# Optimization experiments

Hardware: AMD Instinct MI355X
Metric: run time of the kernel (lower is better)

The kernel has to match this reference:

```python
import jax, jax.numpy as jnp
import numpy as np
import math

D_MODEL = 1024
N_HEADS = 16
C = 1
B, L = 8, 2048


def _glorot(key, fan):
    lim = np.sqrt(6.0 / (fan + fan)).astype(np.float32)
    return jax.random.uniform(key, (fan, fan), jnp.float32, -lim, lim)


def setup_inputs() -> dict:
    key = jax.random.key(0)
    ks = jax.random.split(key, 7)
    queries = jax.random.normal(ks[0], (B, L, D_MODEL), jnp.float32)
    keys = jax.random.normal(ks[1], (B, L, D_MODEL), jnp.float32)
    values = jax.random.normal(ks[2], (B, L, D_MODEL), jnp.float32)
    wq = _glorot(ks[3], D_MODEL)
    wk = _glorot(ks[4], D_MODEL)
    wv = _glorot(ks[5], D_MODEL)
    wo = _glorot(ks[6], D_MODEL)
    return {"queries": queries, "keys": keys, "values": values,
            "wq": wq, "wk": wk, "wv": wv, "wo": wo}


def reference(queries, keys, values, wq, wk, wv, wo):
    Bv, Lv, _ = queries.shape
    H = N_HEADS
    Dh = D_MODEL // N_HEADS
    # Projections, then (B, L, H, Dh) -> (B, H, Dh, L)  (time axis last)
    Q = (queries @ wq).reshape(Bv, Lv, H, Dh).transpose(0, 2, 3, 1)
    K = (keys @ wk).reshape(Bv, Lv, H, Dh).transpose(0, 2, 3, 1)
    V = (values @ wv).reshape(Bv, Lv, H, Dh).transpose(0, 2, 3, 1)
    # FFT-based autocorrelation over the time axis, per (B,H,Dh) lane
    corr = jnp.fft.irfft(jnp.fft.rfft(Q, axis=-1) * jnp.conj(jnp.fft.rfft(K, axis=-1)), n=Lv, axis=-1)  # (B,H,Dh,L)
    k_top = int(math.floor(C * math.log(Lv)))
    top_vals, top_idx = jax.lax.top_k(corr, k_top)          # (B,H,Dh,k)
    w = jax.nn.softmax(top_vals, axis=-1)                    # (B,H,Dh,k)
    # Faithful to original roll_function: it rolls along the Dh axis
    # (which the source mislabels as seq_len), shifts taken mod Dh.
    # out[b,h,t,:] = V[b,h,(t - tau[b,h,t]) % Dh, :]
    t = jnp.arange(Dh)
    out = jnp.zeros_like(V)
    for i in range(k_top):  # small static loop (k_top = 7)
        gather_idx = (t[None, None, :] - top_idx[..., i]) % Dh   # (B,H,Dh)
        rolled = jnp.take_along_axis(V, gather_idx[..., None], axis=2)  # (B,H,Dh,L)
        out = out + w[..., i, None] * rolled
    # Faithful layout-scrambling reshape: (B,H,Dh,L)->(B,Dh,H,L)->(B,L,d_model)
    out = out.transpose(0, 2, 1, 3).reshape(Bv, Lv, D_MODEL)
    return out @ wo
```

## Files before the change

### kernel.cpp

```cpp
#include <hip/hip_runtime.h>
#include <math.h>

#define NB 8
#define NL 2048
#define ND 1024
#define NH 16
#define KTOP 7

typedef __attribute__((ext_vector_type(4))) float f32x4;
typedef __attribute__((ext_vector_type(8))) short s16x8;
typedef __attribute__((ext_vector_type(8))) _Float16 f16x8;
typedef __attribute__((ext_vector_type(4))) _Float16 f16x4;

__device__ __forceinline__ unsigned short f2bf(float x) {
  unsigned u = __float_as_uint(x);
  u = (u + 0x7FFFu + ((u >> 16) & 1u)) >> 16;
  return (unsigned short)u;
}
__device__ __forceinline__ float bf2f(unsigned short h) {
  return __uint_as_float(((unsigned)h) << 16);
}
__device__ __forceinline__ unsigned cvtpk_bf16(float a, float b) {
  unsigned d;
  asm("v_cvt_pk_bf16_f32 %0, %1, %2" : "=v"(d) : "v"(a), "v"(b));
  return d;
}
__device__ __forceinline__ float lo16(unsigned h) { return __uint_as_float(h << 16); }
__device__ __forceinline__ float hi16(unsigned h) { return __uint_as_float(h & 0xffff0000u); }

__device__ __forceinline__ void gll16(const void* g, void* l) {
  __builtin_amdgcn_global_load_lds(
      (const __attribute__((address_space(1))) void*)g,
      (__attribute__((address_space(3))) void*)l, 16, 0, 0);
}

__device__ __forceinline__ void asplit_write(float4 x, float4 y, short* ah, short* al, int wi) {
  unsigned h0 = cvtpk_bf16(x.x, x.y);
  unsigned h1 = cvtpk_bf16(x.z, x.w);
  unsigned h2 = cvtpk_bf16(y.x, y.y);
  unsigned h3 = cvtpk_bf16(y.z, y.w);
  float r0 = x.x - lo16(h0), r1 = x.y - hi16(h0);
  float r2 = x.z - lo16(h1), r3 = x.w - hi16(h1);
  float r4 = y.x - lo16(h2), r5 = y.y - hi16(h2);
  float r6 = y.z - lo16(h3), r7 = y.w - hi16(h3);
  unsigned l0 = cvtpk_bf16(r0, r1);
  unsigned l1 = cvtpk_bf16(r2, r3);
  unsigned l2 = cvtpk_bf16(r4, r5);
  unsigned l3 = cvtpk_bf16(r6, r7);
  *(uint4*)(ah + wi) = make_uint4(h0, h1, h2, h3);
  *(uint4*)(al + wi) = make_uint4(l0, l1, l2, l3);
}

__global__ __launch_bounds__(256) void wprep_kernel(
    const float* __restrict__ w0, const float* __restrict__ w1,
    const float* __restrict__ w2, const float* __restrict__ w3,
    short* __restrict__ wsplit, _Float16* __restrict__ wf16) {
  __shared__ float tile[32][33];
  int y = blockIdx.y;
  const float* in = (y == 0) ? w0 : (y == 1) ? w1 : (y == 2) ? w2 : w3;
  int bx = blockIdx.x & 31, by = blockIdx.x >> 5;
  int tx = threadIdx.x & 31, ty = threadIdx.x >> 5;
#pragma unroll
  for (int i = 0; i < 4; ++i)
    tile[ty + i * 8][tx] = in[(size_t)(by * 32 + ty + i * 8) * ND + bx * 32 + tx];
  __syncthreads();
#pragma unroll
  for (int i = 0; i < 4; ++i) {
    float x = tile[tx][ty + i * 8];
    int n = bx * 32 + ty + i * 8;
    int k = by * 32 + tx;
    if (y < 2) {
      short* oh = wsplit + (size_t)(2 * y) * ND * ND;
      short* ol = wsplit + (size_t)(2 * y + 1) * ND * ND;
      unsigned short h = f2bf(x);
      unsigned short l = f2bf(x - bf2f(h));
      size_t o = (size_t)n * ND + (k ^ (((n >> 1) & 3) << 3));
      oh[o] = (short)h;
      ol[o] = (short)l;
    } else {
      _Float16* of = wf16 + (size_t)(y - 2) * ND * ND;
      of[(size_t)n * ND + (k ^ ((n & 7) << 3))] = (_Float16)x;
    }
  }
}

__global__ __launch_bounds__(256) void gemm_split(
    const float* __restrict__ A, const short* __restrict__ BhT,
    const short* __restrict__ BlT, float* __restrict__ Ct) {
  constexpr int K = 1024;
  __shared__ short smem[32768];
  int t = threadIdx.x;
  int wg = (blockIdx.x & 7) * 128 + (blockIdx.x >> 3);
  int m0 = (wg >> 3) << 7, n0 = (wg & 7) << 7;
  int lane = t & 63;
  int wm = (t >> 7) & 1, wn = (t >> 6) & 1;
  int lrow = lane & 15, lk8 = (lane >> 4) << 3;

  int r0 = t >> 2, r1 = r0 + 64;
  int c8 = (t & 3) << 3;
  int wi0 = r0 * 32 + (c8 ^ (((r0 >> 1) & 3) << 3));
  int wi1 = r1 * 32 + (c8 ^ (((r1 >> 1) & 3) << 3));
  int lo0 = (t & 192) * 8;
  int lo1 = 2048 + (t & 192) * 8;

  const float* pa0 = A + (size_t)(m0 + r0) * K + c8;
  const float* pa1 = A + (size_t)(m0 + r1) * K + c8;
  const short* pb0h = BhT + (size_t)(n0 + r0) * K + c8;
  const short* pb1h = BhT + (size_t)(n0 + r1) * K + c8;
  const short* pb0l = BlT + (size_t)(n0 + r0) * K + c8;
  const short* pb1l = BlT + (size_t)(n0 + r1) * K + c8;

  int iA[4], iB[4];
#pragma unroll
  for (int f = 0; f < 4; ++f) {
    int ra = wm * 64 + f * 16 + lrow;
    iA[f] = ra * 32 + (lk8 ^ (((ra >> 1) & 3) << 3));
    int rb = wn * 64 + f * 16 + lrow;
    iB[f] = rb * 32 + (lk8 ^ (((rb >> 1) & 3) << 3));
  }

  f32x4 acc[4][4] = {};

  float4 sx0 = *(const float4*)(pa0);
  float4 sy0 = *(const float4*)(pa0 + 4);
  float4 sx1 = *(const float4*)(pa1);
  float4 sy1 = *(const float4*)(pa1 + 4);
  gll16(pb0h, smem + 8192 + lo0);
  gll16(pb1h, smem + 8192 + lo1);
  gll16(pb0l, smem + 12288 + lo0);
  gll16(pb1l, smem + 12288 + lo1);
  asplit_write(sx0, sy0, smem, smem + 4096, wi0);
  asplit_write(sx1, sy1, smem, smem + 4096, wi1);
  __syncthreads();

  for (int k0 = 0; k0 < K; k0 += 32) {
    short* cb = smem + ((k0 >> 5) & 1) * 16384;
    short* nb = smem + ((((k0 >> 5) & 1) ^ 1) * 16384);
    bool more = (k0 + 32) < K;
    if (more) {
      sx0 = *(const float4*)(pa0 + k0 + 32);
      sy0 = *(const float4*)(pa0 + k0 + 36);
      sx1 = *(const float4*)(pa1 + k0 + 32);
      sy1 = *(const float4*)(pa1 + k0 + 36);
      gll16(pb0h + k0 + 32, nb + 8192 + lo0);
      gll16(pb1h + k0 + 32, nb + 8192 + lo1);
      gll16(pb0l + k0 + 32, nb + 12288 + lo0);
      gll16(pb1l + k0 + 32, nb + 12288 + lo1);
    }
    s16x8 afh[4], afl[4];
#pragma unroll
    for (int mf = 0; mf < 4; ++mf) {
      afh[mf] = *(const s16x8*)(cb + iA[mf]);
      afl[mf] = *(const s16x8*)(cb + 4096 + iA[mf]);
    }
#pragma unroll
    for (int nf = 0; nf < 4; ++nf) {
      s16x8 bfh = *(const s16x8*)(cb + 8192 + iB[nf]);
      s16x8 bfl = *(const s16x8*)(cb + 12288 + iB[nf]);
#pragma unroll
      for (int mf = 0; mf < 4; ++mf)
        acc[mf][nf] = __builtin_amdgcn_mfma_f32_16x16x32_bf16(afh[mf], bfh, acc[mf][nf], 0, 0, 0);
#pragma unroll
      for (int mf = 0; mf < 4; ++mf)
        acc[mf][nf] = __builtin_amdgcn_mfma_f32_16x16x32_bf16(afh[mf], bfl, acc[mf][nf], 0, 0, 0);
#pragma unroll
      for (int mf = 0; mf < 4; ++mf)
        acc[mf][nf] = __builtin_amdgcn_mfma_f32_16x16x32_bf16(afl[mf], bfh, acc[mf][nf], 0, 0, 0);
    }
    if (more) {
      asplit_write(sx0, sy0, nb, nb + 4096, wi0);
      asplit_write(sx1, sy1, nb, nb + 4096, wi1);
    }
    __syncthreads();
  }

  int b = m0 >> 11;
  int mlbase = (m0 & 2047) + wm * 64 + (lane >> 4) * 4;
#pragma unroll
  for (int nf = 0; nf < 4; ++nf) {
    int n = n0 + wn * 64 + nf * 16 + lrow;
    float* rowp = Ct + ((size_t)(b * ND + n)) * NL + mlbase;
#pragma unroll
    for (int mf = 0; mf < 4; ++mf)
      *(float4*)(rowp + mf * 16) = *(float4*)&acc[mf][nf];
  }
}

template <int OUTMODE, bool AF32>
__global__ __launch_bounds__(256) void gemm_f16(
    const void* __restrict__ Av, const _Float16* __restrict__ BT,
    void* __restrict__ Cv) {
  constexpr int K = 1024;
  __shared__ _Float16 sA[8192];
  __shared__ _Float16 sB[8192];
  int t = threadIdx.x;
  int wg = (blockIdx.x & 7) * 128 + (blockIdx.x >> 3);
  int m0 = (wg >> 3) << 7, n0 = (wg & 7) << 7;
  int lane = t & 63;
  int wm = (t >> 7) & 1, wn = (t >> 6) & 1;
  int lrow = lane & 15, lk = (lane >> 4) << 3;

  f32x4 acc[4][4] = {};

  for (int k0 = 0; k0 < K; k0 += 64) {
#pragma unroll
    for (int it = 0; it < 4; ++it) {
      int e = it * 256 + t;
      int r = e >> 3, c8 = (e & 7) << 3;
      int lo = it * 2048 + (t & 192) * 8;
      gll16(BT + (size_t)(n0 + r) * K + k0 + c8, sB + lo);
      if (!AF32) {
        const _Float16* Af = (const _Float16*)Av;
        gll16(Af + (size_t)(m0 + r) * K + k0 + c8, sA + lo);
      }
    }
    if (AF32) {
      const float* Af = (const float*)Av;
#pragma unroll
      for (int it = 0; it < 4; ++it) {
        int ca = it * 256 + t;
        int r = ca >> 3, c8 = (ca & 7) << 3;
        const float* pa = Af + (size_t)(m0 + r) * K + k0 + c8;
        float4 x = *(const float4*)pa;
        float4 y = *(const float4*)(pa + 4);
        f16x8 o;
        o[0] = (_Float16)x.x; o[1] = (_Float16)x.y; o[2] = (_Float16)x.z; o[3] = (_Float16)x.w;
        o[4] = (_Float16)y.x; o[5] = (_Float16)y.y; o[6] = (_Float16)y.z; o[7] = (_Float16)y.w;
        *(f16x8*)(sA + r * 64 + (c8 ^ ((r & 7) << 3))) = o;
      }
    }
    __syncthreads();
#pragma unroll
    for (int kk = 0; kk < 64; kk += 32) {
      f16x8 af[4];
#pragma unroll
      for (int mf = 0; mf < 4; ++mf) {
        int row = wm * 64 + mf * 16 + lrow;
        af[mf] = *(const f16x8*)(sA + row * 64 + ((kk + lk) ^ ((row & 7) << 3)));
      }
#pragma unroll
      for (int nf = 0; nf < 4; ++nf) {
        int row = wn * 64 + nf * 16 + lrow;
        f16x8 bf = *(const f16x8*)(sB + row * 64 + ((kk + lk) ^ ((row & 7) << 3)));
#pragma unroll
        for (int mf = 0; mf < 4; ++mf)
          acc[mf][nf] = __builtin_amdgcn_mfma_f32_16x16x32_f16(af[mf], bf, acc[mf][nf], 0, 0, 0);
      }
    }
    __syncthreads();
  }

  if (OUTMODE == 0) {
    _Float16* C = (_Float16*)Cv;
    int b = m0 >> 11;
    int ml = (m0 & 2047) + wm * 64 + (lane >> 4) * 4;
#pragma unroll
    for (int nf = 0; nf < 4; ++nf) {
      int n = n0 + wn * 64 + nf * 16 + lrow;
      _Float16* row = C + ((size_t)(b * ND + n)) * NL + ml;
#pragma unroll
      for (int mf = 0; mf < 4; ++mf) {
        f16x4 v;
        v[0] = (_Float16)acc[mf][nf][0];
        v[1] = (_Float16)acc[mf][nf][1];
        v[2] = (_Float16)acc[mf][nf][2];
        v[3] = (_Float16)acc[mf][nf][3];
        *(f16x4*)(row + mf * 16) = v;
      }
    }
  } else {
    float* C = (float*)Cv;
#pragma unroll
    for (int mf = 0; mf < 4; ++mf)
#pragma unroll
      for (int nf = 0; nf < 4; ++nf) {
        int row = m0 + wm * 64 + mf * 16 + (lane >> 4) * 4;
        int col = n0 + wn * 64 + nf * 16 + lrow;
#pragma unroll
        for (int r = 0; r < 4; ++r)
          C[(size_t)(row + r) * ND + col] = acc[mf][nf][r];
      }
  }
}

__device__ __forceinline__ int SW(int i) { return i ^ ((i >> 4) & 7); }

__device__ __forceinline__ float2 cadd2(float2 a, float2 b) { return make_float2(a.x + b.x, a.y + b.y); }
__device__ __forceinline__ float2 csub2(float2 a, float2 b) { return make_float2(a.x - b.x, a.y - b.y); }
__device__ __forceinline__ float2 cmul2(float2 a, float2 b) {
  return make_float2(a.x * b.x - a.y * b.y, a.x * b.y + a.y * b.x);
}
__device__ __forceinline__ float2 cjs2(float2 a, float s) { return make_float2(-s * a.y, s * a.x); }
__device__ __forceinline__ float2 wtw(float rev) {
  return make_float2(__builtin_amdgcn_cosf(rev), __builtin_amdgcn_sinf(rev));
}

__device__ __forceinline__ void dft4(float2& b0, float2& b1, float2& b2, float2& b3, float s) {
  float2 t0 = cadd2(b0, b2), t1 = csub2(b0, b2);
  float2 t2 = cadd2(b1, b3), t3 = cjs2(csub2(b1, b3), s);
  b0 = cadd2(t0, t2);
  b1 = cadd2(t1, t3);
  b2 = csub2(t0, t2);
  b3 = csub2(t1, t3);
}

__device__ __forceinline__ void dft8(float2 a[8], float s) {
  float2 e0 = a[0], e1 = a[2], e2 = a[4], e3 = a[6];
  float2 o0 = a[1], o1 = a[3], o2 = a[5], o3 = a[7];
  dft4(e0, e1, e2, e3, s);
  dft4(o0, o1, o2, o3, s);
  const float c = 0.70710678118654752f;
  float2 w1 = make_float2(c, s * c);
  float2 w3 = make_float2(-c, s * c);
  o1 = cmul2(o1, w1);
  o2 = cjs2(o2, s);
  o3 = cmul2(o3, w3);
  a[0] = cadd2(e0, o0);
  a[4] = csub2(e0, o0);
  a[1] = cadd2(e1, o1);
  a[5] = csub2(e1, o1);
  a[2] = cadd2(e2, o2);
  a[6] = csub2(e2, o2);
  a[3] = cadd2(e3, o3);
  a[7] = csub2(e3, o3);
}

template <int LS>
__device__ __forceinline__ void pass8(const float2* __restrict__ in, float2* __restrict__ out,
                                      float s, int t) {
  float2 a[8];
  const float2* ip = in + (t ^ ((t >> 4) & 7));
#pragma unroll
  for (int r = 0; r < 8; ++r) a[r] = ip[256 * r];
  int k = t & (LS - 1);
  if (LS > 1) {
    float kf = s * (1.0f / (LS * 8)) * (float)k;
    float2 w1 = wtw(kf);
    float2 w4 = wtw(4.0f * kf);
    float2 w2 = cmul2(w1, w1);
    float2 w3 = cmul2(w2, w1);
    float2 w5 = cmul2(w4, w1);
    float2 w6 = cmul2(w4, w2);
    float2 w7 = cmul2(w4, w3);
    a[1] = cmul2(a[1], w1);
    a[2] = cmul2(a[2], w2);
    a[3] = cmul2(a[3], w3);
    a[4] = cmul2(a[4], w4);
    a[5] = cmul2(a[5], w5);
    a[6] = cmul2(a[6], w6);
    a[7] = cmul2(a[7], w7);
  }
  dft8(a, s);
  int ob = (t / LS) * (LS * 8) + k;
#pragma unroll
  for (int r = 0; r < 8; ++r) out[SW(ob + LS * r)] = a[r];
}

__global__ __launch_bounds__(256) void fft_topk_kernel(
    const float* __restrict__ Qt, const float* __restrict__ Kt,
    float* __restrict__ topw, int* __restrict__ topi) {
  __shared__ float2 X[2048];
  __shared__ float2 Y[2048];
  __shared__ float cv[2][4];
  __shared__ int ct[2][4];

  int t = threadIdx.x;
  size_t rix = blockIdx.x;
  const float* q = Qt + rix * NL;
  const float* k = Kt + rix * NL;

#pragma unroll
  for (int it = 0; it < 2; ++it) {
    int i0 = 4 * t + 1024 * it;
    float4 vq = *(const float4*)(q + i0);
    float4 vk = *(const float4*)(k + i0);
    int swb = SW(i0);
    X[swb ^ 0] = make_float2(vq.x, vk.x);
    X[swb ^ 1] = make_float2(vq.y, vk.y);
    X[swb ^ 2] = make_float2(vq.z, vk.z);
    X[swb ^ 3] = make_float2(vq.w, vk.w);
  }
  __syncthreads();

  pass8<1>(X, Y, -1.0f, t);
  __syncthreads();
  pass8<8>(Y, X, -1.0f, t);
  __syncthreads();
  pass8<64>(X, Y, -1.0f, t);
  __syncthreads();
#pragma unroll
  for (int h = 0; h < 2; ++h) {
    int b = t + 256 * h;
    float2 a[4];
    const float2* yp = Y + SW(b);
#pragma unroll
    for (int r = 0; r < 4; ++r) a[r] = yp[512 * r];
    float2 w = wtw(-(1.0f / 2048.0f) * (float)b);
    float2 w2 = cmul2(w, w);
    a[1] = cmul2(a[1], w);
    a[2] = cmul2(a[2], w2);
    a[3] = cmul2(a[3], cmul2(w2, w));
    dft4(a[0], a[1], a[2], a[3], -1.0f);
    float2* xp = X + SW(b);
#pragma unroll
    for (int r = 0; r < 4; ++r) xp[512 * r] = a[r];
  }
  __syncthreads();

#pragma unroll
  for (int it = 0; it < 8; ++it) {
    int f = t + 256 * it;
    int nf = (2048 - f) & 2047;
    float2 zf = X[SW(t) + 256 * it];
    float2 zn = X[SW(nf)];
    float a = zf.x, b2 = zf.y, c = zn.x, d = zn.y;
    float p = 0.5f * (a + c), qq = 0.5f * (b2 - d);
    float r2 = 0.5f * (b2 + d), s2 = -0.5f * (a - c);
    Y[SW(t) + 256 * it] = make_float2((p * r2 + qq * s2) * (1.0f / 2048.0f),
                                      (qq * r2 - p * s2) * (1.0f / 2048.0f));
  }
  __syncthreads();

  pass8<1>(Y, X, 1.0f, t);
  __syncthreads();
  pass8<8>(X, Y, 1.0f, t);
  __syncthreads();
  pass8<64>(Y, X, 1.0f, t);
  __syncthreads();

  float lv[8];
  int lt[8];
#pragma unroll
  for (int h = 0; h < 2; ++h) {
    int b = t + 256 * h;
    float2 a[4];
    const float2* xp = X + SW(b);
#pragma unroll
    for (int r = 0; r < 4; ++r) a[r] = xp[512 * r];
    float2 w = wtw((1.0f / 2048.0f) * (float)b);
    float2 w2 = cmul2(w, w);
    a[1] = cmul2(a[1], w);
    a[2] = cmul2(a[2], w2);
    a[3] = cmul2(a[3], cmul2(w2, w));
    dft4(a[0], a[1], a[2], a[3], 1.0f);
#pragma unroll
    for (int r = 0; r < 4; ++r) {
      lv[h * 4 + r] = a[r].x;
      lt[h * 4 + r] = b + 512 * r;
    }
  }

  int lane = t & 63, wave = t >> 6;
  float bv = lv[0];
  int bt = lt[0];
#pragma unroll
  for (int j = 1; j < 8; ++j)
    if (lv[j] > bv) { bv = lv[j]; bt = lt[j]; }

  float sel_v[KTOP];
  int sel_t[KTOP];
#pragma unroll
  for (int pass = 0; pass < KTOP; ++pass) {
    float rv = bv;
    int rt = bt;
#pragma unroll
    for (int m = 1; m < 64; m <<= 1) {
      float ov = __shfl_xor(rv, m, 64);
      int ot = __shfl_xor(rt, m, 64);
      if (ov > rv) { rv = ov; rt = ot; }
    }
    if (lane == 0) { cv[pass & 1][wave] = rv; ct[pass & 1][wave] = rt; }
    __syncthreads();
    float fv = cv[pass & 1][0];
    int ft = ct[pass & 1][0];
#pragma unroll
    for (int w = 1; w < 4; ++w) {
      float ov = cv[pass & 1][w];
      if (ov > fv) { fv = ov; ft = ct[pass & 1][w]; }
    }
    sel_v[pass] = fv;
    sel_t[pass] = ft;
    if (bt == ft) {
#pragma unroll
      for (int j = 0; j < 8; ++j)
        if (lt[j] == ft) lv[j] = -3.0e38f;
      bv = lv[0];
      bt = lt[0];
#pragma unroll
      for (int j = 1; j < 8; ++j)
        if (lv[j] > bv) { bv = lv[j]; bt = lt[j]; }
    }
  }

  if (t == 0) {
    float m = sel_v[0], ssum = 0.f, w[KTOP];
#pragma unroll
    for (int i = 0; i < KTOP; ++i) { w[i] = expf(sel_v[i] - m); ssum += w[i]; }
#pragma unroll
    for (int i = 0; i < KTOP; ++i) {
      topw[rix * KTOP + i] = w[i] / ssum;
      topi[rix * KTOP + i] = sel_t[i];
    }
  }
}

__global__ __launch_bounds__(256) void roll_kernel(
    const _Float16* __restrict__ V, const float* __restrict__ topw,
    const int* __restrict__ topi, _Float16* __restrict__ out) {
  __shared__ float vt[64][68];
  __shared__ float ws[64][8];
  __shared__ int ts[64][8];
  int blk = blockIdx.x;
  int b = blk >> 9;
  int h = (blk >> 5) & 15;
  int lc = blk & 31;
  int t = threadIdx.x;

#pragma unroll
  for (int it = 0; it < 2; ++it) {
    int e = it * 256 + t;
    int d = e >> 3, c8 = (e & 7) << 3;
    f16x8 v = *(const f16x8*)(V + ((size_t)(b * ND + h * 64 + d)) * NL + lc * 64 + c8);
#pragma unroll
    for (int j = 0; j < 8; ++j) vt[d][c8 + j] = (float)v[j];
  }
  for (int e = t; e < 64 * KTOP; e += 256) {
    int d = e / KTOP, i = e % KTOP;
    size_t rix = ((size_t)(b * 16 + h)) * 64 + d;
    ws[d][i] = topw[rix * KTOP + i];
    ts[d][i] = topi[rix * KTOP + i] & 63;
  }
  __syncthreads();

  int hi = lc >> 4;
  int c0 = (lc & 15) * 64;
#pragma unroll
  for (int it = 0; it < 16; ++it) {
    int e = it * 256 + t;
    int d = e >> 6, r = e & 63;
    float s = 0.f;
#pragma unroll
    for (int i = 0; i < KTOP; ++i) s += ws[d][i] * vt[(d - ts[d][i]) & 63][r];
    int rowp = d * 32 + h * 2 + hi;
    int col = c0 + r;
    out[((size_t)(b * NL + rowp)) * ND + (col ^ ((rowp & 7) << 3))] = (_Float16)s;
  }
}

extern "C" void kernel_launch(void* const* d_in, const int* in_sizes, int n_in,
                              void* d_out, int out_size, void* d_ws, size_t ws_size,
                              hipStream_t stream) {
  (void)in_sizes; (void)n_in; (void)out_size; (void)ws_size;
  const float* queries = (const float*)d_in[0];
  const float* keys    = (const float*)d_in[1];
  const float* values  = (const float*)d_in[2];
  const float* wq = (const float*)d_in[3];
  const float* wk = (const float*)d_in[4];
  const float* wv = (const float*)d_in[5];
  const float* wo = (const float*)d_in[6];
  float* outp = (float*)d_out;

  const size_t MB = 1024 * 1024;
  char* ws = (char*)d_ws;
  short*    wsplit = (short*)ws;
  _Float16* wf16   = (_Float16*)(ws + 8 * MB);
  float*    Qt     = (float*)(ws + 12 * MB);
  float*    Kt     = (float*)(ws + 76 * MB);
  float*    topw   = (float*)(ws + 140 * MB);
  int*      topi   = (int*)(ws + 140 * MB + (size_t)8192 * KTOP * 4);

  short* wqh = wsplit + (size_t)0 * ND * ND;
  short* wql = wsplit + (size_t)1 * ND * ND;
  short* wkh = wsplit + (size_t)2 * ND * ND;
  short* wkl = wsplit + (size_t)3 * ND * ND;
  _Float16* wv16 = wf16 + (size_t)0 * ND * ND;
  _Float16* wo16 = wf16 + (size_t)1 * ND * ND;

  _Float16* Vp = (_Float16*)Qt;
  _Float16* Xs = (_Float16*)Kt;

  wprep_kernel<<<dim3(1024, 4), 256, 0, stream>>>(wq, wk, wv, wo, wsplit, wf16);

  gemm_split<<<1024, 256, 0, stream>>>(queries, wqh, wql, Qt);
  gemm_split<<<1024, 256, 0, stream>>>(keys, wkh, wkl, Kt);

  fft_topk_kernel<<<8192, 256, 0, stream>>>(Qt, Kt, topw, topi);

  gemm_f16<0, true><<<1024, 256, 0, stream>>>(values, wv16, Vp);

  roll_kernel<<<NB * NH * 32, 256, 0, stream>>>(Vp, topw, topi, Xs);

  gemm_f16<2, false><<<1024, 256, 0, stream>>>(Xs, wo16, outp);
}
```

Measured before the change: 467.1 us.

## Double-buffer GEMM shared-memory tiles and fuse spectrum product into first FFT pass

The f16 GEMM kernel now ping-pongs between two shared-memory stages. The next K-tile's global loads (and, for fp32 A, the register-held values converted after the MFMAs) are issued while the current tile is being multiplied, and one barrier per iteration is dropped. Shared memory grows to 64 KB per block, which may reduce occupancy. Separately, the FFT correlation kernel computes the conjugate-product spectrum straight into registers and applies the first radix-8 pass in place, removing one LDS round trip and one barrier.

```diff
diff --git a/kernel.cpp b/kernel.cpp
--- a/kernel.cpp
+++ b/kernel.cpp
@@ -191,8 +191,7 @@
     const void* __restrict__ Av, const _Float16* __restrict__ BT,
     void* __restrict__ Cv) {
   constexpr int K = 1024;
-  __shared__ _Float16 sA[8192];
-  __shared__ _Float16 sB[8192];
+  __shared__ _Float16 smem[32768];
   int t = threadIdx.x;
   int wg = (blockIdx.x & 7) * 128 + (blockIdx.x >> 3);
   int m0 = (wg >> 3) << 7, n0 = (wg & 7) << 7;
@@ -200,51 +199,93 @@
   int wm = (t >> 7) & 1, wn = (t >> 6) & 1;
   int lrow = lane & 15, lk = (lane >> 4) << 3;
 
+  int rs = t >> 3;
+  int c8 = (t & 7) << 3;
+  const _Float16* pB[4];
+  const float* pAf[4];
+  const _Float16* pAh[4];
+  int wiA[4], lo[4];
+#pragma unroll
+  for (int it = 0; it < 4; ++it) {
+    int r = it * 32 + rs;
+    pB[it] = BT + (size_t)(n0 + r) * K + c8;
+    lo[it] = it * 2048 + (t & 192) * 8;
+    if (AF32) {
+      pAf[it] = (const float*)Av + (size_t)(m0 + r) * K + c8;
+      wiA[it] = r * 64 + (c8 ^ ((r & 7) << 3));
+    } else {
+      pAh[it] = (const _Float16*)Av + (size_t)(m0 + r) * K + c8;
+    }
+  }
+
   f32x4 acc[4][4] = {};
+  float4 ax[4], ay[4];
+
+#pragma unroll
+  for (int it = 0; it < 4; ++it) {
+    gll16(pB[it], smem + 8192 + lo[it]);
+    if (!AF32) {
+      gll16(pAh[it], smem + lo[it]);
+    } else {
+      ax[it] = *(const float4*)(pAf[it]);
+      ay[it] = *(const float4*)(pAf[it] + 4);
+    }
+  }
+  if (AF32) {
+#pragma unroll
+    for (int it = 0; it < 4; ++it) {
+      f16x8 o;
+      o[0] = (_Float16)ax[it].x; o[1] = (_Float16)ax[it].y;
+      o[2] = (_Float16)ax[it].z; o[3] = (_Float16)ax[it].w;
+      o[4] = (_Float16)ay[it].x; o[5] = (_Float16)ay[it].y;
+      o[6] = (_Float16)ay[it].z; o[7] = (_Float16)ay[it].w;
+      *(f16x8*)(smem + wiA[it]) = o;
+    }
+  }
+  __syncthreads();
 
   for (int k0 = 0; k0 < K; k0 += 64) {
-#pragma unroll
-    for (int it = 0; it < 4; ++it) {
-      int e = it * 256 + t;
-      int r = e >> 3, c8 = (e & 7) << 3;
-      int lo = it * 2048 + (t & 192) * 8;
-      gll16(BT + (size_t)(n0 + r) * K + k0 + c8, sB + lo);
-      if (!AF32) {
-        const _Float16* Af = (const _Float16*)Av;
-        gll16(Af + (size_t)(m0 + r) * K + k0 + c8, sA + lo);
+    _Float16* cb = smem + ((k0 >> 6) & 1) * 16384;
+    _Float16* nb = smem + ((((k0 >> 6) & 1) ^ 1) * 16384);
+    bool more = (k0 + 64) < K;
+    if (more) {
+#pragma unroll
+      for (int it = 0; it < 4; ++it) {
+        gll16(pB[it] + k0 + 64, nb + 8192 + lo[it]);
+        if (!AF32) {
+          gll16(pAh[it] + k0 + 64, nb + lo[it]);
+        } else {
+          ax[it] = *(const float4*)(pAf[it] + k0 + 64);
+          ay[it] = *(const float4*)(pAf[it] + k0 + 68);
+        }
       }
     }
-    if (AF32) {
-      const float* Af = (const float*)Av;
-#pragma unroll
-      for (int it = 0; it < 4; ++it) {
-        int ca = it * 256 + t;
-        int r = ca >> 3, c8 = (ca & 7) << 3;
-        const float* pa = Af + (size_t)(m0 + r) * K + k0 + c8;
-        float4 x = *(const float4*)pa;
-        float4 y = *(const float4*)(pa + 4);
-        f16x8 o;
-        o[0] = (_Float16)x.x; o[1] = (_Float16)x.y; o[2] = (_Float16)x.z; o[3] = (_Float16)x.w;
-        o[4] = (_Float16)y.x; o[5] = (_Float16)y.y; o[6] = (_Float16)y.z; o[7] = (_Float16)y.w;
-        *(f16x8*)(sA + r * 64 + (c8 ^ ((r & 7) << 3))) = o;
-      }
-    }
-    __syncthreads();
 #pragma unroll
     for (int kk = 0; kk < 64; kk += 32) {
       f16x8 af[4];
 #pragma unroll
       for (int mf = 0; mf < 4; ++mf) {
         int row = wm * 64 + mf * 16 + lrow;
-        af[mf] = *(const f16x8*)(sA + row * 64 + ((kk + lk) ^ ((row & 7) << 3)));
+        af[mf] = *(const f16x8*)(cb + row * 64 + ((kk + lk) ^ ((row & 7) << 3)));
       }
 #pragma unroll
       for (int nf = 0; nf < 4; ++nf) {
         int row = wn * 64 + nf * 16 + lrow;
-        f16x8 bf = *(const f16x8*)(sB + row * 64 + ((kk + lk) ^ ((row & 7) << 3)));
+        f16x8 bf = *(const f16x8*)(cb + 8192 + row * 64 + ((kk + lk) ^ ((row & 7) << 3)));
 #pragma unroll
         for (int mf = 0; mf < 4; ++mf)
           acc[mf][nf] = __builtin_amdgcn_mfma_f32_16x16x32_f16(af[mf], bf, acc[mf][nf], 0, 0, 0);
+      }
+    }
+    if (more && AF32) {
+#pragma unroll
+      for (int it = 0; it < 4; ++it) {
+        f16x8 o;
+        o[0] = (_Float16)ax[it].x; o[1] = (_Float16)ax[it].y;
+        o[2] = (_Float16)ax[it].z; o[3] = (_Float16)ax[it].w;
+        o[4] = (_Float16)ay[it].x; o[5] = (_Float16)ay[it].y;
+        o[6] = (_Float16)ay[it].z; o[7] = (_Float16)ay[it].w;
+        *(f16x8*)(nb + wiA[it]) = o;
       }
     }
     __syncthreads();
@@ -407,25 +448,31 @@
   }
   __syncthreads();
 
-#pragma unroll
-  for (int it = 0; it < 8; ++it) {
-    int f = t + 256 * it;
-    int nf = (2048 - f) & 2047;
-    float2 zf = X[SW(t) + 256 * it];
-    float2 zn = X[SW(nf)];
-    float a = zf.x, b2 = zf.y, c = zn.x, d = zn.y;
-    float p = 0.5f * (a + c), qq = 0.5f * (b2 - d);
-    float r2 = 0.5f * (b2 + d), s2 = -0.5f * (a - c);
-    Y[SW(t) + 256 * it] = make_float2((p * r2 + qq * s2) * (1.0f / 2048.0f),
-                                      (qq * r2 - p * s2) * (1.0f / 2048.0f));
-  }
-  __syncthreads();
-
-  pass8<1>(Y, X, 1.0f, t);
-  __syncthreads();
-  pass8<8>(X, Y, 1.0f, t);
-  __syncthreads();
-  pass8<64>(Y, X, 1.0f, t);
+  {
+    float2 a[8];
+    int swt = SW(t);
+#pragma unroll
+    for (int r = 0; r < 8; ++r) {
+      int f = t + 256 * r;
+      int nf = (2048 - f) & 2047;
+      float2 zf = X[swt + 256 * r];
+      float2 zn = X[SW(nf)];
+      float aa = zf.x, b2 = zf.y, c = zn.x, d = zn.y;
+      float p = 0.5f * (aa + c), qq = 0.5f * (b2 - d);
+      float r2 = 0.5f * (b2 + d), s2 = -0.5f * (aa - c);
+      a[r] = make_float2((p * r2 + qq * s2) * (1.0f / 2048.0f),
+                         (qq * r2 - p * s2) * (1.0f / 2048.0f));
+    }
+    dft8(a, 1.0f);
+    int ob = t * 8;
+#pragma unroll
+    for (int r = 0; r < 8; ++r) Y[SW(ob + r)] = a[r];
+  }
+  __syncthreads();
+
+  pass8<8>(Y, X, 1.0f, t);
+  __syncthreads();
+  pass8<64>(X, Y, 1.0f, t);
   __syncthreads();
 
   float lv[8];
@@ -434,9 +481,9 @@
   for (int h = 0; h < 2; ++h) {
     int b = t + 256 * h;
     float2 a[4];
-    const float2* xp = X + SW(b);
-#pragma unroll
-    for (int r = 0; r < 4; ++r) a[r] = xp[512 * r];
+    const float2* yp = Y + SW(b);
+#pragma unroll
+    for (int r = 0; r < 4; ++r) a[r] = yp[512 * r];
     float2 w = wtw((1.0f / 2048.0f) * (float)b);
     float2 w2 = cmul2(w, w);
     a[1] = cmul2(a[1], w);
```

Result: faster. 457.5 us (-2.0%).
